# Kernel optimization log

Hardware: AMD Instinct MI355X
Metric: run time of the kernel (lower is better)

## Reference

```python
import jax, jax.numpy as jnp
import numpy as np


def setup_inputs() -> dict:
    key = jax.random.key(0)
    ks = jax.random.split(key, 7)
    B, D, d1, d2, d3 = 256, 256, 1024, 512, 256
    s = lambda f: 1.0 / np.sqrt(f)  # torch nn.Linear-style init scale
    return {
        "x": jax.random.normal(ks[0], (B, D), jnp.float32),
        "W1": jax.random.normal(ks[1], (d1, D), jnp.float32) * s(D),
        "b1": jax.random.normal(ks[2], (d1,), jnp.float32) * s(D),
        "W2": jax.random.normal(ks[3], (d2, d1), jnp.float32) * s(d1),
        "b2": jax.random.normal(ks[4], (d2,), jnp.float32) * s(d1),
        "W3": jax.random.normal(ks[5], (d3, d2), jnp.float32) * s(d2),
        "b3": jax.random.normal(ks[6], (d3,), jnp.float32) * s(d2),
        "k": 10,
    }


def _border_dists(x, W1, b1, W2, b2, W3, b3):
    # Layer 1: pre-activations and boundary distances. For the first layer the
    # effective linear map is W1 itself (shared across the batch).
    z1 = x @ W1.T + b1                                   # [B, d1]
    dist1 = jnp.abs(z1) / jnp.linalg.norm(W1, axis=1)    # [B, d1]
    m1 = (z1 > 0).astype(x.dtype)
    V1 = m1[:, :, None] * W1[None]                       # [B, d1, D] per-instance map after ReLU
    h1 = m1 * z1

    # Layer 2
    z2 = h1 @ W2.T + b2                                  # [B, d2]
    V2 = jnp.einsum('oi,bid->bod', W2, V1)               # [B, d2, D]
    dist2 = jnp.abs(z2) / jnp.linalg.norm(V2, axis=2)
    m2 = (z2 > 0).astype(x.dtype)
    h2 = m2 * z2

    # Layer 3
    z3 = h2 @ W3.T + b3                                  # [B, d3]
    V3 = jnp.einsum('oi,bid->bod', W3, m2[:, :, None] * V2)  # [B, d3, D]
    dist3 = jnp.abs(z3) / jnp.linalg.norm(V3, axis=2)

    return jnp.concatenate([dist1, dist2, dist3], axis=1)  # [B, d1+d2+d3]


def reference(x, W1, b1, W2, b2, W3, b3, k):
    dists = _border_dists(x, W1, b1, W2, b2, W3, b3)
    # smallest-k distances per instance via top_k on negated distances
    neg_top, _ = jax.lax.top_k(-dists, k)                # [B, k]
    return jnp.sum(-neg_top)                             # border-distance loss (scalar)
```

## Files before the change

kernel.cpp:

```cpp
#include <hip/hip_runtime.h>
#include <math.h>
#include <float.h>

#define B   256
#define D   256
#define D1  1024
#define D2  512
#define D3  256
#define NDIST (D1 + D2 + D3)
#define CQ  2.0f

typedef __attribute__((ext_vector_type(8))) short short8;
typedef __attribute__((ext_vector_type(4))) float f32x4;
typedef __attribute__((ext_vector_type(4))) int   i32x4;

__device__ __forceinline__ float waveReduceSum(float v) {
    #pragma unroll
    for (int off = 32; off > 0; off >>= 1)
        v += __shfl_down(v, off, 64);
    return v;
}
__device__ __forceinline__ float waveReduceMax(float v) {
    #pragma unroll
    for (int off = 32; off > 0; off >>= 1)
        v = fmaxf(v, __shfl_down(v, off, 64));
    return v;
}

__device__ __forceinline__ unsigned short f2bf(float f) {
    unsigned int u = __float_as_uint(f);
    u = (u + 0x7FFFu + ((u >> 16) & 1u)) >> 16;
    return (unsigned short)u;
}
__device__ __forceinline__ float bf2f(unsigned short h) {
    return __uint_as_float(((unsigned int)h) << 16);
}
__device__ __forceinline__ void gld16(const void* g, void* l) {
    __builtin_amdgcn_global_load_lds(
        (const __attribute__((address_space(1))) unsigned int*)g,
        (__attribute__((address_space(3))) unsigned int*)l, 16, 0, 0);
}

__device__ __forceinline__ int swz_src(int row, int lane) {
    return ((lane & 3) + ((row >> 1) & 3)) & 3;
}
__device__ __forceinline__ int swz_frag(int row, int quad) {
    return row * 32 + (((quad - ((row >> 1) & 3)) & 3) * 8);
}

__global__ __launch_bounds__(256) void k_prep(
    const float* __restrict__ x,  const float* __restrict__ W1,
    const float* __restrict__ W2, const float* __restrict__ W3,
    float* __restrict__ zeros,
    float* __restrict__ outp,
    unsigned short* __restrict__ xhi,  unsigned short* __restrict__ xlo,
    unsigned short* __restrict__ W1hi, unsigned short* __restrict__ W1lo,
    unsigned short* __restrict__ W2hi, unsigned short* __restrict__ W2lo,
    unsigned short* __restrict__ W3hi, unsigned short* __restrict__ W3lo,
    signed char* __restrict__ W1Ti8, float* __restrict__ saq,
    signed char* __restrict__ W2i8,  float* __restrict__ sbq,
    signed char* __restrict__ W3i8,  float* __restrict__ s3q,
    float* __restrict__ rn1) {
    int blk = blockIdx.x;
    int t = threadIdx.x;
    if (blk < 1536) {
        if (blk == 0 && t == 0) outp[0] = 0.f;
        zeros[blk * 256 + t] = 0.f;
        return;
    }
    if (blk < 2496) {
        int i4 = ((blk - 1536) * 256 + t) * 4;
        const float* src; unsigned short *hi, *lo; int off;
        if (i4 < 65536)       { src = x;  hi = xhi;  lo = xlo;  off = i4; }
        else if (i4 < 327680) { src = W1; hi = W1hi; lo = W1lo; off = i4 - 65536; }
        else if (i4 < 851968) { src = W2; hi = W2hi; lo = W2lo; off = i4 - 327680; }
        else                  { src = W3; hi = W3hi; lo = W3lo; off = i4 - 851968; }
        float4 v = *(const float4*)(src + off);
        ushort4 h, l;
        h.x = f2bf(v.x); l.x = f2bf(v.x - bf2f(h.x));
        h.y = f2bf(v.y); l.y = f2bf(v.y - bf2f(h.y));
        h.z = f2bf(v.z); l.z = f2bf(v.z - bf2f(h.z));
        h.w = f2bf(v.w); l.w = f2bf(v.w - bf2f(h.w));
        *(ushort4*)(hi + off) = h;
        *(ushort4*)(lo + off) = l;
        return;
    }
    if (blk < 2528) {
        int ty = t >> 5, tx = t & 31;
        int d = (blk - 2496) * 8 + ty;
        float m = 0.f;
        for (int i = tx; i < D1; i += 32) m = fmaxf(m, fabsf(W1[(size_t)i * D + d]));
        #pragma unroll
        for (int off = 16; off > 0; off >>= 1) m = fmaxf(m, __shfl_down(m, off, 32));
        m = __shfl(m, 0, 32);
        m = fmaxf(m, 1e-20f);
        if (tx == 0) saq[d] = m / 127.f;
        float inv = 127.f / m;
        for (int i = tx; i < D1; i += 32) {
            int q = __float2int_rn(W1[(size_t)i * D + d] * inv);
            W1Ti8[(size_t)d * D1 + i] = (signed char)q;
        }
        return;
    }
    if (blk < 2656) {
        int o = (blk - 2528) * 4 + (t >> 6);
        int l = t & 63;
        const float* row = W2 + (size_t)o * D1;
        float m = 0.f;
        for (int tt = l; tt < D1; tt += 64) m = fmaxf(m, fabsf(row[tt]));
        m = waveReduceMax(m);
        m = __shfl(m, 0, 64);
        m = fmaxf(m, 1e-20f);
        if (l == 0) sbq[o] = m / 127.f;
        float inv = 127.f / m;
        for (int tt = l; tt < D1; tt += 64)
            W2i8[(size_t)o * D1 + tt] = (signed char)__float2int_rn(row[tt] * inv);
        return;
    }
    if (blk < 2720) {
        int p = (blk - 2656) * 4 + (t >> 6);
        int l = t & 63;
        const float* row = W3 + (size_t)p * D2;
        float m = 0.f;
        for (int tt = l; tt < D2; tt += 64) m = fmaxf(m, fabsf(row[tt]));
        m = waveReduceMax(m);
        m = __shfl(m, 0, 64);
        m = fmaxf(m, 1e-20f);
        if (l == 0) s3q[p] = m / 127.f;
        float inv = 127.f / m;
        for (int tt = l; tt < D2; tt += 64)
            W3i8[(size_t)p * D2 + tt] = (signed char)__float2int_rn(row[tt] * inv);
        return;
    }
    {
        int gw = (blk - 2720) * 4 + (t >> 6);
        int lane = t & 63;
        const float* row = W1 + (size_t)gw * D;
        float s = 0.f;
        for (int tt = lane; tt < D; tt += 64) { float v = row[tt]; s += v * v; }
        s = waveReduceSum(s);
        if (lane == 0) rn1[gw] = sqrtf(s);
    }
}

template <int KD, int KL>
__device__ __forceinline__ void mfma3_64(
    const unsigned short* __restrict__ Ahi, const unsigned short* __restrict__ Alo,
    const unsigned short* __restrict__ Bhi, const unsigned short* __restrict__ Blo,
    int m0, int n0, int k0, unsigned short* sm, f32x4 acc[2][2]) {
    int tid = threadIdx.x;
    int l = tid & 63, w = tid >> 6;
    int rsub = l >> 2;
    int quad = l >> 4, l16 = l & 15;
    int wm = (w >> 1) * 32, wn = (w & 1) * 32;
    unsigned short* sAh = sm;
    unsigned short* sAl = sm + 2048;
    unsigned short* sBh = sm + 4096;
    unsigned short* sBl = sm + 6144;
    ptrdiff_t dA = Alo - Ahi, dB = Blo - Bhi;
    int rloc = w * 16 + rsub;
    int c = swz_src(rloc, l);
    const unsigned short* pa = Ahi + (size_t)(m0 + rloc) * KD + k0 + c * 8;
    const unsigned short* pb = Bhi + (size_t)(n0 + rloc) * KD + k0 + c * 8;
    int aoff[2], boff[2];
    #pragma unroll
    for (int mt = 0; mt < 2; mt++) aoff[mt] = swz_frag(wm + mt * 16 + l16, quad);
    #pragma unroll
    for (int nt = 0; nt < 2; nt++) boff[nt] = swz_frag(wn + nt * 16 + l16, quad);
    for (int kk = 0; kk < KL; kk += 32) {
        gld16(pa + kk,      sAh + w * 512);
        gld16(pa + dA + kk, sAl + w * 512);
        gld16(pb + kk,      sBh + w * 512);
        gld16(pb + dB + kk, sBl + w * 512);
        __syncthreads();
        short8 ah[2], al[2], bh[2], bl[2];
        #pragma unroll
        for (int mt = 0; mt < 2; mt++) {
            ah[mt] = *(const short8*)(sAh + aoff[mt]);
            al[mt] = *(const short8*)(sAl + aoff[mt]);
        }
        #pragma unroll
        for (int nt = 0; nt < 2; nt++) {
            bh[nt] = *(const short8*)(sBh + boff[nt]);
            bl[nt] = *(const short8*)(sBl + boff[nt]);
        }
        #pragma unroll
        for (int mt = 0; mt < 2; mt++)
            #pragma unroll
            for (int nt = 0; nt < 2; nt++) {
                acc[mt][nt] = __builtin_amdgcn_mfma_f32_16x16x32_bf16(ah[mt], bh[nt], acc[mt][nt], 0, 0, 0);
                acc[mt][nt] = __builtin_amdgcn_mfma_f32_16x16x32_bf16(ah[mt], bl[nt], acc[mt][nt], 0, 0, 0);
                acc[mt][nt] = __builtin_amdgcn_mfma_f32_16x16x32_bf16(al[mt], bh[nt], acc[mt][nt], 0, 0, 0);
            }
        __syncthreads();
    }
}

__global__ __launch_bounds__(256) void k_l1(
    const unsigned short* __restrict__ xhi,  const unsigned short* __restrict__ xlo,
    const unsigned short* __restrict__ W1hi, const unsigned short* __restrict__ W1lo,
    const float* __restrict__ b1, const float* __restrict__ rn1,
    float* __restrict__ dists, unsigned char* __restrict__ m1q,
    unsigned short* __restrict__ h1hi, unsigned short* __restrict__ h1lo) {
    __shared__ __align__(16) unsigned short sm[8192];
    int m0 = blockIdx.x * 64, n0 = blockIdx.y * 64;
    f32x4 acc[2][2] = {};
    mfma3_64<D, D>(xhi, xlo, W1hi, W1lo, m0, n0, 0, sm, acc);
    int l = threadIdx.x & 63, w = threadIdx.x >> 6;
    int quad = l >> 4, l16 = l & 15;
    int wm = (w >> 1) * 32, wn = (w & 1) * 32;
    #pragma unroll
    for (int mt = 0; mt < 2; mt++)
        #pragma unroll
        for (int nt = 0; nt < 2; nt++) {
            int n = n0 + wn + nt * 16 + l16;
            float bv = b1[n], rv = rn1[n];
            #pragma unroll
            for (int r = 0; r < 4; r++) {
                int m = m0 + wm + mt * 16 + quad * 4 + r;
                float z = acc[mt][nt][r] + bv;
                size_t idx = (size_t)m * D1 + n;
                dists[idx] = fabsf(z) / rv;
                m1q[idx] = (z > 0.f) ? 0xFFu : 0u;
                float h = z > 0.f ? z : 0.f;
                unsigned short hh = f2bf(h);
                h1hi[idx] = hh;
                h1lo[idx] = f2bf(h - bf2f(hh));
            }
        }
}

__global__ __launch_bounds__(256) void k_l2a(
    const unsigned short* __restrict__ h1hi, const unsigned short* __restrict__ h1lo,
    const unsigned short* __restrict__ W2hi, const unsigned short* __restrict__ W2lo,
    float* __restrict__ z2) {
    __shared__ __align__(16) unsigned short sm[8192];
    int m0 = blockIdx.x * 64, n0 = blockIdx.y * 64, k0 = blockIdx.z * 256;
    f32x4 acc[2][2] = {};
    mfma3_64<D1, 256>(h1hi, h1lo, W2hi, W2lo, m0, n0, k0, sm, acc);
    int l = threadIdx.x & 63, w = threadIdx.x >> 6;
    int quad = l >> 4, l16 = l & 15;
    int wm = (w >> 1) * 32, wn = (w & 1) * 32;
    #pragma unroll
    for (int mt = 0; mt < 2; mt++)
        #pragma unroll
        for (int nt = 0; nt < 2; nt++) {
            int n = n0 + wn + nt * 16 + l16;
            #pragma unroll
            for (int r = 0; r < 4; r++) {
                int m = m0 + wm + mt * 16 + quad * 4 + r;
                atomicAdd(&z2[(size_t)m * D2 + n], acc[mt][nt][r]);
            }
        }
}

__global__ __launch_bounds__(256) void k_l2b(
    const float* __restrict__ b2, float* __restrict__ z2,
    unsigned char* __restrict__ m2q,
    unsigned short* __restrict__ h2hi, unsigned short* __restrict__ h2lo) {
    int idx = blockIdx.x * 256 + threadIdx.x;
    int n = idx & (D2 - 1);
    float z = z2[idx] + b2[n];
    z2[idx] = z;
    m2q[idx] = (z > 0.f) ? 0xFFu : 0u;
    float h = z > 0.f ? z : 0.f;
    unsigned short hh = f2bf(h);
    h2hi[idx] = hh;
    h2lo[idx] = f2bf(h - bf2f(hh));
}

__global__ __launch_bounds__(256) void k_l3a(
    const unsigned short* __restrict__ h2hi, const unsigned short* __restrict__ h2lo,
    const unsigned short* __restrict__ W3hi, const unsigned short* __restrict__ W3lo,
    float* __restrict__ z3) {
    __shared__ __align__(16) unsigned short sm[8192];
    int m0 = blockIdx.x * 64, n0 = blockIdx.y * 64, k0 = blockIdx.z * 256;
    f32x4 acc[2][2] = {};
    mfma3_64<D2, 256>(h2hi, h2lo, W3hi, W3lo, m0, n0, k0, sm, acc);
    int l = threadIdx.x & 63, w = threadIdx.x >> 6;
    int quad = l >> 4, l16 = l & 15;
    int wm = (w >> 1) * 32, wn = (w & 1) * 32;
    #pragma unroll
    for (int mt = 0; mt < 2; mt++)
        #pragma unroll
        for (int nt = 0; nt < 2; nt++) {
            int n = n0 + wn + nt * 16 + l16;
            #pragma unroll
            for (int r = 0; r < 4; r++) {
                int m = m0 + wm + mt * 16 + quad * 4 + r;
                atomicAdd(&z3[(size_t)m * D3 + n], acc[mt][nt][r]);
            }
        }
}

__global__ __launch_bounds__(256) void k_l3b(
    const float* __restrict__ b3, float* __restrict__ z3) {
    int idx = blockIdx.x * 256 + threadIdx.x;
    z3[idx] = z3[idx] + b3[idx & (D3 - 1)];
}

__global__ __launch_bounds__(256) void k_gemm1(
    const signed char* __restrict__ W1Ti8,
    const signed char* __restrict__ W2i8,
    const unsigned char* __restrict__ m1q,
    const float* __restrict__ saq,
    const float* __restrict__ sbq,
    signed char* __restrict__ qV2,
    float* __restrict__ norm2,
    int b0) {
    __shared__ __align__(16) signed char As[16384];
    __shared__ __align__(16) signed char Bs[16384];
    int m0 = blockIdx.x * 128;
    int o0 = blockIdx.y * 128;
    int bc = blockIdx.z;
    int b = b0 + bc;
    int tid = threadIdx.x;
    int l = tid & 63, w = tid >> 6;
    int quad = l >> 4, l16 = l & 15;
    int wm = (w >> 1) * 64, wn = (w & 1) * 64;
    const unsigned char* mrow = m1q + (size_t)b * D1;

    const signed char* pa[4];
    const signed char* pb[4];
    int lrow = l >> 3, ls = l & 7;
    #pragma unroll
    for (int r = 0; r < 4; r++) {
        int row = r * 32 + w * 8 + lrow;
        int c = (ls + (row & 7)) & 7;
        pa[r] = W1Ti8 + (size_t)(m0 + row) * D1 + c * 16;
        pb[r] = W2i8 + (size_t)(o0 + row) * D1 + c * 16;
    }
    int aoff[4][2], boff[4][2];
    #pragma unroll
    for (int mt = 0; mt < 4; mt++) {
        int tr = wm + mt * 16 + l16;
        #pragma unroll
        for (int ks = 0; ks < 2; ks++)
            aoff[mt][ks] = tr * 128 + (((ks * 4 + quad) - (tr & 7)) & 7) * 16;
    }
    #pragma unroll
    for (int nt = 0; nt < 4; nt++) {
        int tr = wn + nt * 16 + l16;
        #pragma unroll
        for (int ks = 0; ks < 2; ks++)
            boff[nt][ks] = tr * 128 + (((ks * 4 + quad) - (tr & 7)) & 7) * 16;
    }

    i32x4 acc[4][4];
    #pragma unroll
    for (int i = 0; i < 4; i++)
        #pragma unroll
        for (int j = 0; j < 4; j++) acc[i][j] = (i32x4)0;

    for (int kk = 0; kk < D1; kk += 128) {
        #pragma unroll
        for (int r = 0; r < 4; r++) {
            gld16(pa[r] + kk, As + r * 4096 + w * 1024);
            gld16(pb[r] + kk, Bs + r * 4096 + w * 1024);
        }
        i32x4 mv0 = *(const i32x4*)(mrow + kk + quad * 16);
        i32x4 mv1 = *(const i32x4*)(mrow + kk + 64 + quad * 16);
        __syncthreads();
        #pragma unroll
        for (int ks = 0; ks < 2; ks++) {
            i32x4 mv = ks ? mv1 : mv0;
            i32x4 a[4], bq[4];
            #pragma unroll
            for (int mt = 0; mt < 4; mt++)
                a[mt] = (*(const i32x4*)(As + aoff[mt][ks])) & mv;
            #pragma unroll
            for (int nt = 0; nt < 4; nt++)
                bq[nt] = *(const i32x4*)(Bs + boff[nt][ks]);
            #pragma unroll
            for (int mt = 0; mt < 4; mt++)
                #pragma unroll
                for (int nt = 0; nt < 4; nt++)
                    acc[mt][nt] = __builtin_amdgcn_mfma_i32_16x16x64_i8(
                        a[mt], bq[nt], acc[mt][nt], 0, 0, 0);
        }
        __syncthreads();
    }

    float sad[4][4];
    #pragma unroll
    for (int mt = 0; mt < 4; mt++)
        #pragma unroll
        for (int r = 0; r < 4; r++)
            sad[mt][r] = saq[m0 + wm + mt * 16 + quad * 4 + r];
    float sbv[4], sbdq[4];
    #pragma unroll
    for (int nt = 0; nt < 4; nt++) {
        sbv[nt] = sbq[o0 + wn + nt * 16 + l16];
        sbdq[nt] = sbv[nt] * (1.0f / CQ);
    }

    #pragma unroll
    for (int nt = 0; nt < 4; nt++) {
        float s = 0.f;
        #pragma unroll
        for (int mt = 0; mt < 4; mt++)
            #pragma unroll
            for (int r = 0; r < 4; r++) {
                float v = (float)acc[mt][nt][r] * sad[mt][r] * sbv[nt];
                s += v * v;
            }
        s += __shfl_down(s, 32, 64);
        s += __shfl_down(s, 16, 64);
        if (l < 16)
            atomicAdd(&norm2[(size_t)b * D2 + o0 + wn + nt * 16 + l], s);
    }

    signed char* qb = qV2 + (size_t)bc * (D * D2);
    #pragma unroll
    for (int mt = 0; mt < 4; mt++) {
        int dbase = m0 + wm + mt * 16 + quad * 4;
        #pragma unroll
        for (int r = 0; r < 4; r++)
            #pragma unroll
            for (int nt = 0; nt < 4; nt++) {
                int o = o0 + wn + nt * 16 + l16;
                int qi = __float2int_rn((float)acc[mt][nt][r] * sbdq[nt]);
                qi = max(-127, min(127, qi));
                qb[(size_t)(dbase + r) * D2 + o] = (signed char)qi;
            }
    }
}

__global__ __launch_bounds__(256) void k_gemm2(
    const signed char* __restrict__ W3i8,
    const signed char* __restrict__ qV2,
    const unsigned char* __restrict__ m2q,
    const float* __restrict__ saq,
    const float* __restrict__ s3q,
    float* __restrict__ norm3,
    int b0) {
    __shared__ __align__(16) signed char As[16384];
    __shared__ __align__(16) signed char Bs[16384];
    int m0 = blockIdx.x * 128;
    int n0 = blockIdx.y * 128;
    int bc = blockIdx.z;
    int b = b0 + bc;
    int tid = threadIdx.x;
    int l = tid & 63, w = tid >> 6;
    int quad = l >> 4, l16 = l & 15;
    int wm = (w >> 1) * 64, wn = (w & 1) * 64;
    const unsigned char* mrow = m2q + (size_t)b * D2;
    const signed char* Bsrc = qV2 + (size_t)bc * (D * D2);

    const signed char* pa[4];
    const signed char* pb[4];
    int lrow = l >> 3, ls = l & 7;
    #pragma unroll
    for (int r = 0; r < 4; r++) {
        int row = r * 32 + w * 8 + lrow;
        int c = (ls + (row & 7)) & 7;
        pa[r] = W3i8 + (size_t)(m0 + row) * D2 + c * 16;
        pb[r] = Bsrc + (size_t)(n0 + row) * D2 + c * 16;
    }
    int aoff[4][2], boff[4][2];
    #pragma unroll
    for (int mt = 0; mt < 4; mt++) {
        int tr = wm + mt * 16 + l16;
        #pragma unroll
        for (int ks = 0; ks < 2; ks++)
            aoff[mt][ks] = tr * 128 + (((ks * 4 + quad) - (tr & 7)) & 7) * 16;
    }
    #pragma unroll
    for (int nt = 0; nt < 4; nt++) {
        int tr = wn + nt * 16 + l16;
        #pragma unroll
        for (int ks = 0; ks < 2; ks++)
            boff[nt][ks] = tr * 128 + (((ks * 4 + quad) - (tr & 7)) & 7) * 16;
    }

    i32x4 acc[4][4];
    #pragma unroll
    for (int i = 0; i < 4; i++)
        #pragma unroll
        for (int j = 0; j < 4; j++) acc[i][j] = (i32x4)0;

    for (int kk = 0; kk < D2; kk += 128) {
        #pragma unroll
        for (int r = 0; r < 4; r++) {
            gld16(pa[r] + kk, As + r * 4096 + w * 1024);
            gld16(pb[r] + kk, Bs + r * 4096 + w * 1024);
        }
        i32x4 mv0 = *(const i32x4*)(mrow + kk + quad * 16);
        i32x4 mv1 = *(const i32x4*)(mrow + kk + 64 + quad * 16);
        __syncthreads();
        #pragma unroll
        for (int ks = 0; ks < 2; ks++) {
            i32x4 mv = ks ? mv1 : mv0;
            i32x4 a[4], bq[4];
            #pragma unroll
            for (int mt = 0; mt < 4; mt++)
                a[mt] = *(const i32x4*)(As + aoff[mt][ks]);
            #pragma unroll
            for (int nt = 0; nt < 4; nt++)
                bq[nt] = (*(const i32x4*)(Bs + boff[nt][ks])) & mv;
            #pragma unroll
            for (int mt = 0; mt < 4; mt++)
                #pragma unroll
                for (int nt = 0; nt < 4; nt++)
                    acc[mt][nt] = __builtin_amdgcn_mfma_i32_16x16x64_i8(
                        a[mt], bq[nt], acc[mt][nt], 0, 0, 0);
        }
        __syncthreads();
    }

    float saCQ[4];
    #pragma unroll
    for (int nt = 0; nt < 4; nt++)
        saCQ[nt] = saq[n0 + wn + nt * 16 + l16] * CQ;

    #pragma unroll
    for (int mt = 0; mt < 4; mt++)
        #pragma unroll
        for (int r = 0; r < 4; r++) {
            float s = 0.f;
            #pragma unroll
            for (int nt = 0; nt < 4; nt++) {
                float v = (float)acc[mt][nt][r] * saCQ[nt];
                s += v * v;
            }
            s += __shfl_down(s, 8, 64);
            s += __shfl_down(s, 4, 64);
            s += __shfl_down(s, 2, 64);
            s += __shfl_down(s, 1, 64);
            if (l16 == 0) {
                int p = m0 + wm + mt * 16 + quad * 4 + r;
                float s3 = s3q[p];
                atomicAdd(&norm3[(size_t)b * D3 + p], s * s3 * s3);
            }
        }
}

__global__ __launch_bounds__(256) void k_topk(
    const float* __restrict__ dists,
    const float* __restrict__ z2, const float* __restrict__ norm2,
    const float* __restrict__ z3, const float* __restrict__ norm3,
    const int* __restrict__ kp, float* __restrict__ outp) {
    __shared__ unsigned long long wmin[4];
    int b = blockIdx.x, t = threadIdx.x;
    float lv[7];
    #pragma unroll
    for (int j = 0; j < 4; j++) lv[j] = dists[(size_t)b * D1 + t + 256 * j];
    #pragma unroll
    for (int j = 4; j < 6; j++) {
        int o = t + 256 * j - 1024;
        lv[j] = fabsf(z2[(size_t)b * D2 + o]) / sqrtf(norm2[(size_t)b * D2 + o]);
    }
    lv[6] = fabsf(z3[(size_t)b * D3 + t]) / sqrtf(norm3[(size_t)b * D3 + t]);
    int k = *kp;
    if (k > NDIST) k = NDIST;
    float sum = 0.f;
    for (int it = 0; it < k; it++) {
        float mv = lv[0]; int mj = 0;
        #pragma unroll
        for (int j = 1; j < 7; j++)
            if (lv[j] < mv) { mv = lv[j]; mj = j; }
        unsigned long long key =
            ((unsigned long long)__float_as_uint(mv) << 32) | (unsigned)(t * 8 + mj);
        #pragma unroll
        for (int off = 32; off > 0; off >>= 1) {
            unsigned long long o = __shfl_down(key, off, 64);
            if (o < key) key = o;
        }
        if ((t & 63) == 0) wmin[t >> 6] = key;
        __syncthreads();
        unsigned long long k0 = wmin[0];
        #pragma unroll
        for (int ww = 1; ww < 4; ww++) if (wmin[ww] < k0) k0 = wmin[ww];
        sum += __uint_as_float((unsigned)(k0 >> 32));
        int wt = (int)((k0 & 0xFFFu) >> 3), wj = (int)(k0 & 7u);
        if (t == wt) lv[wj] = FLT_MAX;
        __syncthreads();
    }
    if (t == 0) atomicAdd(outp, sum);
}

extern "C" void kernel_launch(void* const* d_in, const int* in_sizes, int n_in,
                              void* d_out, int out_size, void* d_ws, size_t ws_size,
                              hipStream_t stream) {
    const float* x  = (const float*)d_in[0];
    const float* W1 = (const float*)d_in[1];
    const float* b1 = (const float*)d_in[2];
    const float* W2 = (const float*)d_in[3];
    const float* b2 = (const float*)d_in[4];
    const float* W3 = (const float*)d_in[5];
    const float* b3 = (const float*)d_in[6];
    const int*   kp = (const int*)d_in[7];
    float* outp = (float*)d_out;

    float* fp = (float*)d_ws;
    float* rn1     = fp;                          fp += D1;
    float* dists   = fp;                          fp += (size_t)B * D1;
    float* saq     = fp;                          fp += D;
    float* sbq     = fp;                          fp += D2;
    float* s3q     = fp;                          fp += D3;
    float* z2      = fp;                          fp += (size_t)B * D2;
    float* z3      = fp;                          fp += (size_t)B * D3;
    float* norm2   = fp;                          fp += (size_t)B * D2;
    float* norm3   = fp;                          fp += (size_t)B * D3;
    unsigned short* up = (unsigned short*)fp;
    unsigned short* W2hi  = up;  up += (size_t)D2 * D1;
    unsigned short* W2lo  = up;  up += (size_t)D2 * D1;
    unsigned short* W3hi  = up;  up += (size_t)D3 * D2;
    unsigned short* W3lo  = up;  up += (size_t)D3 * D2;
    unsigned short* xhi   = up;  up += (size_t)B * D;
    unsigned short* xlo   = up;  up += (size_t)B * D;
    unsigned short* W1hi  = up;  up += (size_t)D1 * D;
    unsigned short* W1lo  = up;  up += (size_t)D1 * D;
    unsigned short* h1hi  = up;  up += (size_t)B * D1;
    unsigned short* h1lo  = up;  up += (size_t)B * D1;
    unsigned short* h2hi  = up;  up += (size_t)B * D2;
    unsigned short* h2lo  = up;  up += (size_t)B * D2;
    signed char*    cp = (signed char*)up;
    signed char*    W1Ti8 = cp;  cp += (size_t)D * D1;
    signed char*    W2i8  = cp;  cp += (size_t)D2 * D1;
    signed char*    W3i8  = cp;  cp += (size_t)D3 * D2;
    unsigned char*  m1q   = (unsigned char*)cp;  cp += (size_t)B * D1;
    unsigned char*  m2q   = (unsigned char*)cp;  cp += (size_t)B * D2;
    signed char*    qV2   = cp;

    size_t base_bytes = (size_t)((char*)qV2 - (char*)d_ws);
    int CH = 8;
    const int cands[6] = {256, 128, 64, 32, 16, 8};
    for (int c = 0; c < 6; c++) {
        size_t need = base_bytes + (size_t)cands[c] * D * D2;
        if (need <= ws_size) { CH = cands[c]; break; }
    }

    k_prep<<<2976, 256, 0, stream>>>(x, W1, W2, W3, z2, outp,
                                     xhi, xlo, W1hi, W1lo, W2hi, W2lo, W3hi, W3lo,
                                     W1Ti8, saq, W2i8, sbq, W3i8, s3q, rn1);

    k_l1<<<dim3(B / 64, D1 / 64), 256, 0, stream>>>(xhi, xlo, W1hi, W1lo, b1, rn1,
                                                    dists, m1q, h1hi, h1lo);
    k_l2a<<<dim3(B / 64, D2 / 64, 4), 256, 0, stream>>>(h1hi, h1lo, W2hi, W2lo, z2);
    k_l2b<<<(B * D2) / 256, 256, 0, stream>>>(b2, z2, m2q, h2hi, h2lo);
    k_l3a<<<dim3(B / 64, D3 / 64, 2), 256, 0, stream>>>(h2hi, h2lo, W3hi, W3lo, z3);
    k_l3b<<<(B * D3) / 256, 256, 0, stream>>>(b3, z3);

    for (int b0 = 0; b0 < B; b0 += CH) {
        k_gemm1<<<dim3(D / 128, D2 / 128, CH), 256, 0, stream>>>(
            W1Ti8, W2i8, m1q, saq, sbq, qV2, norm2, b0);
        k_gemm2<<<dim3(D3 / 128, D / 128, CH), 256, 0, stream>>>(
            W3i8, qV2, m2q, saq, s3q, norm3, b0);
    }

    k_topk<<<B, 256, 0, stream>>>(dists, z2, norm2, z3, norm3, kp, outp);
}
```

Before: 192.4 us.

## Fuse all stages into one cooperative persistent kernel with grid syncs

Replaces the sequence of separate kernel launches (prep, layer GEMMs, bias passes, chunked int8 V-GEMMs, top-k) with a single cooperative kernel that loops over job indices and separates stages with grid-wide syncs. It also co-schedules independent work in the same phase (gemm1 with l2a, gemm2 with l3a), folds the l3b bias add into top-k, and drops the batch chunking of qV2 by assuming the workspace holds all 256 batches. This is meant to remove launch gaps and tail idling, at the cost of grid-sync overhead, a fixed grid size tied to occupancy, and heavier register pressure from merging all paths into one kernel.

```diff
diff --git a/kernel.cpp b/kernel.cpp
--- a/kernel.cpp
+++ b/kernel.cpp
@@ -1,6 +1,9 @@
 #include <hip/hip_runtime.h>
+#include <hip/hip_cooperative_groups.h>
 #include <math.h>
 #include <float.h>
+
+namespace cg = cooperative_groups;
 
 #define B   256
 #define D   256
@@ -14,6 +17,19 @@
 typedef __attribute__((ext_vector_type(4))) float f32x4;
 typedef __attribute__((ext_vector_type(4))) int   i32x4;
 
+struct KArgs {
+    const float *x, *W1, *b1, *W2, *b2, *W3, *b3;
+    const int* kp;
+    float* outp;
+    float *rn1, *dists, *saq, *sbq, *s3q;
+    float *z2, *z3, *norm2, *norm3;
+    unsigned short *W2hi, *W2lo, *W3hi, *W3lo, *xhi, *xlo, *W1hi, *W1lo;
+    unsigned short *h1hi, *h1lo, *h2hi, *h2lo;
+    signed char *W1Ti8, *W2i8, *W3i8;
+    unsigned char *m1q, *m2q;
+    signed char* qV2;
+};
+
 __device__ __forceinline__ float waveReduceSum(float v) {
     #pragma unroll
     for (int off = 32; off > 0; off >>= 1)
@@ -26,7 +42,6 @@
         v = fmaxf(v, __shfl_down(v, off, 64));
     return v;
 }
-
 __device__ __forceinline__ unsigned short f2bf(float f) {
     unsigned int u = __float_as_uint(f);
     u = (u + 0x7FFFu + ((u >> 16) & 1u)) >> 16;
@@ -40,7 +55,6 @@
         (const __attribute__((address_space(1))) unsigned int*)g,
         (__attribute__((address_space(3))) unsigned int*)l, 16, 0, 0);
 }
-
 __device__ __forceinline__ int swz_src(int row, int lane) {
     return ((lane & 3) + ((row >> 1) & 3)) & 3;
 }
@@ -48,33 +62,20 @@
     return row * 32 + (((quad - ((row >> 1) & 3)) & 3) * 8);
 }
 
-__global__ __launch_bounds__(256) void k_prep(
-    const float* __restrict__ x,  const float* __restrict__ W1,
-    const float* __restrict__ W2, const float* __restrict__ W3,
-    float* __restrict__ zeros,
-    float* __restrict__ outp,
-    unsigned short* __restrict__ xhi,  unsigned short* __restrict__ xlo,
-    unsigned short* __restrict__ W1hi, unsigned short* __restrict__ W1lo,
-    unsigned short* __restrict__ W2hi, unsigned short* __restrict__ W2lo,
-    unsigned short* __restrict__ W3hi, unsigned short* __restrict__ W3lo,
-    signed char* __restrict__ W1Ti8, float* __restrict__ saq,
-    signed char* __restrict__ W2i8,  float* __restrict__ sbq,
-    signed char* __restrict__ W3i8,  float* __restrict__ s3q,
-    float* __restrict__ rn1) {
-    int blk = blockIdx.x;
+__device__ void job_prep(const KArgs& A, int blk) {
     int t = threadIdx.x;
     if (blk < 1536) {
-        if (blk == 0 && t == 0) outp[0] = 0.f;
-        zeros[blk * 256 + t] = 0.f;
+        if (blk == 0 && t == 0) A.outp[0] = 0.f;
+        A.z2[blk * 256 + t] = 0.f;
         return;
     }
     if (blk < 2496) {
         int i4 = ((blk - 1536) * 256 + t) * 4;
         const float* src; unsigned short *hi, *lo; int off;
-        if (i4 < 65536)       { src = x;  hi = xhi;  lo = xlo;  off = i4; }
-        else if (i4 < 327680) { src = W1; hi = W1hi; lo = W1lo; off = i4 - 65536; }
-        else if (i4 < 851968) { src = W2; hi = W2hi; lo = W2lo; off = i4 - 327680; }
-        else                  { src = W3; hi = W3hi; lo = W3lo; off = i4 - 851968; }
+        if (i4 < 65536)       { src = A.x;  hi = A.xhi;  lo = A.xlo;  off = i4; }
+        else if (i4 < 327680) { src = A.W1; hi = A.W1hi; lo = A.W1lo; off = i4 - 65536; }
+        else if (i4 < 851968) { src = A.W2; hi = A.W2hi; lo = A.W2lo; off = i4 - 327680; }
+        else                  { src = A.W3; hi = A.W3hi; lo = A.W3lo; off = i4 - 851968; }
         float4 v = *(const float4*)(src + off);
         ushort4 h, l;
         h.x = f2bf(v.x); l.x = f2bf(v.x - bf2f(h.x));
@@ -89,57 +90,57 @@
         int ty = t >> 5, tx = t & 31;
         int d = (blk - 2496) * 8 + ty;
         float m = 0.f;
-        for (int i = tx; i < D1; i += 32) m = fmaxf(m, fabsf(W1[(size_t)i * D + d]));
+        for (int i = tx; i < D1; i += 32) m = fmaxf(m, fabsf(A.W1[(size_t)i * D + d]));
         #pragma unroll
         for (int off = 16; off > 0; off >>= 1) m = fmaxf(m, __shfl_down(m, off, 32));
         m = __shfl(m, 0, 32);
         m = fmaxf(m, 1e-20f);
-        if (tx == 0) saq[d] = m / 127.f;
+        if (tx == 0) A.saq[d] = m / 127.f;
         float inv = 127.f / m;
         for (int i = tx; i < D1; i += 32) {
-            int q = __float2int_rn(W1[(size_t)i * D + d] * inv);
-            W1Ti8[(size_t)d * D1 + i] = (signed char)q;
+            int q = __float2int_rn(A.W1[(size_t)i * D + d] * inv);
+            A.W1Ti8[(size_t)d * D1 + i] = (signed char)q;
         }
         return;
     }
     if (blk < 2656) {
         int o = (blk - 2528) * 4 + (t >> 6);
         int l = t & 63;
-        const float* row = W2 + (size_t)o * D1;
+        const float* row = A.W2 + (size_t)o * D1;
         float m = 0.f;
         for (int tt = l; tt < D1; tt += 64) m = fmaxf(m, fabsf(row[tt]));
         m = waveReduceMax(m);
         m = __shfl(m, 0, 64);
         m = fmaxf(m, 1e-20f);
-        if (l == 0) sbq[o] = m / 127.f;
+        if (l == 0) A.sbq[o] = m / 127.f;
         float inv = 127.f / m;
         for (int tt = l; tt < D1; tt += 64)
-            W2i8[(size_t)o * D1 + tt] = (signed char)__float2int_rn(row[tt] * inv);
+            A.W2i8[(size_t)o * D1 + tt] = (signed char)__float2int_rn(row[tt] * inv);
         return;
     }
     if (blk < 2720) {
         int p = (blk - 2656) * 4 + (t >> 6);
         int l = t & 63;
-        const float* row = W3 + (size_t)p * D2;
+        const float* row = A.W3 + (size_t)p * D2;
         float m = 0.f;
         for (int tt = l; tt < D2; tt += 64) m = fmaxf(m, fabsf(row[tt]));
         m = waveReduceMax(m);
         m = __shfl(m, 0, 64);
         m = fmaxf(m, 1e-20f);
-        if (l == 0) s3q[p] = m / 127.f;
+        if (l == 0) A.s3q[p] = m / 127.f;
         float inv = 127.f / m;
         for (int tt = l; tt < D2; tt += 64)
-            W3i8[(size_t)p * D2 + tt] = (signed char)__float2int_rn(row[tt] * inv);
+            A.W3i8[(size_t)p * D2 + tt] = (signed char)__float2int_rn(row[tt] * inv);
         return;
     }
     {
         int gw = (blk - 2720) * 4 + (t >> 6);
         int lane = t & 63;
-        const float* row = W1 + (size_t)gw * D;
+        const float* row = A.W1 + (size_t)gw * D;
         float s = 0.f;
         for (int tt = lane; tt < D; tt += 64) { float v = row[tt]; s += v * v; }
         s = waveReduceSum(s);
-        if (lane == 0) rn1[gw] = sqrtf(s);
+        if (lane == 0) A.rn1[gw] = sqrtf(s);
     }
 }
 
@@ -196,16 +197,10 @@
     }
 }
 
-__global__ __launch_bounds__(256) void k_l1(
-    const unsigned short* __restrict__ xhi,  const unsigned short* __restrict__ xlo,
-    const unsigned short* __restrict__ W1hi, const unsigned short* __restrict__ W1lo,
-    const float* __restrict__ b1, const float* __restrict__ rn1,
-    float* __restrict__ dists, unsigned char* __restrict__ m1q,
-    unsigned short* __restrict__ h1hi, unsigned short* __restrict__ h1lo) {
-    __shared__ __align__(16) unsigned short sm[8192];
-    int m0 = blockIdx.x * 64, n0 = blockIdx.y * 64;
+__device__ void job_l1(const KArgs& A, int j, unsigned short* sm) {
+    int m0 = (j & 3) * 64, n0 = (j >> 2) * 64;
     f32x4 acc[2][2] = {};
-    mfma3_64<D, D>(xhi, xlo, W1hi, W1lo, m0, n0, 0, sm, acc);
+    mfma3_64<D, D>(A.xhi, A.xlo, A.W1hi, A.W1lo, m0, n0, 0, sm, acc);
     int l = threadIdx.x & 63, w = threadIdx.x >> 6;
     int quad = l >> 4, l16 = l & 15;
     int wm = (w >> 1) * 32, wn = (w & 1) * 32;
@@ -214,30 +209,26 @@
         #pragma unroll
         for (int nt = 0; nt < 2; nt++) {
             int n = n0 + wn + nt * 16 + l16;
-            float bv = b1[n], rv = rn1[n];
+            float bv = A.b1[n], rv = A.rn1[n];
             #pragma unroll
             for (int r = 0; r < 4; r++) {
                 int m = m0 + wm + mt * 16 + quad * 4 + r;
                 float z = acc[mt][nt][r] + bv;
                 size_t idx = (size_t)m * D1 + n;
-                dists[idx] = fabsf(z) / rv;
-                m1q[idx] = (z > 0.f) ? 0xFFu : 0u;
+                A.dists[idx] = fabsf(z) / rv;
+                A.m1q[idx] = (z > 0.f) ? 0xFFu : 0u;
                 float h = z > 0.f ? z : 0.f;
                 unsigned short hh = f2bf(h);
-                h1hi[idx] = hh;
-                h1lo[idx] = f2bf(h - bf2f(hh));
-            }
-        }
-}
-
-__global__ __launch_bounds__(256) void k_l2a(
-    const unsigned short* __restrict__ h1hi, const unsigned short* __restrict__ h1lo,
-    const unsigned short* __restrict__ W2hi, const unsigned short* __restrict__ W2lo,
-    float* __restrict__ z2) {
-    __shared__ __align__(16) unsigned short sm[8192];
-    int m0 = blockIdx.x * 64, n0 = blockIdx.y * 64, k0 = blockIdx.z * 256;
+                A.h1hi[idx] = hh;
+                A.h1lo[idx] = f2bf(h - bf2f(hh));
+            }
+        }
+}
+
+__device__ void job_l2a(const KArgs& A, int bx, int by, int bz, unsigned short* sm) {
+    int m0 = bx * 64, n0 = by * 64, k0 = bz * 256;
     f32x4 acc[2][2] = {};
-    mfma3_64<D1, 256>(h1hi, h1lo, W2hi, W2lo, m0, n0, k0, sm, acc);
+    mfma3_64<D1, 256>(A.h1hi, A.h1lo, A.W2hi, A.W2lo, m0, n0, k0, sm, acc);
     int l = threadIdx.x & 63, w = threadIdx.x >> 6;
     int quad = l >> 4, l16 = l & 15;
     int wm = (w >> 1) * 32, wn = (w & 1) * 32;
@@ -249,34 +240,27 @@
             #pragma unroll
             for (int r = 0; r < 4; r++) {
                 int m = m0 + wm + mt * 16 + quad * 4 + r;
-                atomicAdd(&z2[(size_t)m * D2 + n], acc[mt][nt][r]);
-            }
-        }
-}
-
-__global__ __launch_bounds__(256) void k_l2b(
-    const float* __restrict__ b2, float* __restrict__ z2,
-    unsigned char* __restrict__ m2q,
-    unsigned short* __restrict__ h2hi, unsigned short* __restrict__ h2lo) {
-    int idx = blockIdx.x * 256 + threadIdx.x;
+                atomicAdd(&A.z2[(size_t)m * D2 + n], acc[mt][nt][r]);
+            }
+        }
+}
+
+__device__ void job_l2b(const KArgs& A, int j) {
+    int idx = j * 256 + threadIdx.x;
     int n = idx & (D2 - 1);
-    float z = z2[idx] + b2[n];
-    z2[idx] = z;
-    m2q[idx] = (z > 0.f) ? 0xFFu : 0u;
+    float z = A.z2[idx] + A.b2[n];
+    A.z2[idx] = z;
+    A.m2q[idx] = (z > 0.f) ? 0xFFu : 0u;
     float h = z > 0.f ? z : 0.f;
     unsigned short hh = f2bf(h);
-    h2hi[idx] = hh;
-    h2lo[idx] = f2bf(h - bf2f(hh));
-}
-
-__global__ __launch_bounds__(256) void k_l3a(
-    const unsigned short* __restrict__ h2hi, const unsigned short* __restrict__ h2lo,
-    const unsigned short* __restrict__ W3hi, const unsigned short* __restrict__ W3lo,
-    float* __restrict__ z3) {
-    __shared__ __align__(16) unsigned short sm[8192];
-    int m0 = blockIdx.x * 64, n0 = blockIdx.y * 64, k0 = blockIdx.z * 256;
+    A.h2hi[idx] = hh;
+    A.h2lo[idx] = f2bf(h - bf2f(hh));
+}
+
+__device__ void job_l3a(const KArgs& A, int bx, int by, int bz, unsigned short* sm) {
+    int m0 = bx * 64, n0 = by * 64, k0 = bz * 256;
     f32x4 acc[2][2] = {};
-    mfma3_64<D2, 256>(h2hi, h2lo, W3hi, W3lo, m0, n0, k0, sm, acc);
+    mfma3_64<D2, 256>(A.h2hi, A.h2lo, A.W3hi, A.W3lo, m0, n0, k0, sm, acc);
     int l = threadIdx.x & 63, w = threadIdx.x >> 6;
     int quad = l >> 4, l16 = l & 15;
     int wm = (w >> 1) * 32, wn = (w & 1) * 32;
@@ -288,37 +272,22 @@
             #pragma unroll
             for (int r = 0; r < 4; r++) {
                 int m = m0 + wm + mt * 16 + quad * 4 + r;
-                atomicAdd(&z3[(size_t)m * D3 + n], acc[mt][nt][r]);
-            }
-        }
-}
-
-__global__ __launch_bounds__(256) void k_l3b(
-    const float* __restrict__ b3, float* __restrict__ z3) {
-    int idx = blockIdx.x * 256 + threadIdx.x;
-    z3[idx] = z3[idx] + b3[idx & (D3 - 1)];
-}
-
-__global__ __launch_bounds__(256) void k_gemm1(
-    const signed char* __restrict__ W1Ti8,
-    const signed char* __restrict__ W2i8,
-    const unsigned char* __restrict__ m1q,
-    const float* __restrict__ saq,
-    const float* __restrict__ sbq,
-    signed char* __restrict__ qV2,
-    float* __restrict__ norm2,
-    int b0) {
-    __shared__ __align__(16) signed char As[16384];
-    __shared__ __align__(16) signed char Bs[16384];
-    int m0 = blockIdx.x * 128;
-    int o0 = blockIdx.y * 128;
-    int bc = blockIdx.z;
-    int b = b0 + bc;
+                atomicAdd(&A.z3[(size_t)m * D3 + n], acc[mt][nt][r]);
+            }
+        }
+}
+
+__device__ void job_gemm1(const KArgs& A, int bx, int by, int bc, signed char* smem) {
+    signed char* As = smem;
+    signed char* Bs = smem + 16384;
+    int m0 = bx * 128;
+    int o0 = by * 128;
+    int b = bc;
     int tid = threadIdx.x;
     int l = tid & 63, w = tid >> 6;
     int quad = l >> 4, l16 = l & 15;
     int wm = (w >> 1) * 64, wn = (w & 1) * 64;
-    const unsigned char* mrow = m1q + (size_t)b * D1;
+    const unsigned char* mrow = A.m1q + (size_t)b * D1;
 
     const signed char* pa[4];
     const signed char* pb[4];
@@ -327,8 +296,8 @@
     for (int r = 0; r < 4; r++) {
         int row = r * 32 + w * 8 + lrow;
         int c = (ls + (row & 7)) & 7;
-        pa[r] = W1Ti8 + (size_t)(m0 + row) * D1 + c * 16;
-        pb[r] = W2i8 + (size_t)(o0 + row) * D1 + c * 16;
+        pa[r] = A.W1Ti8 + (size_t)(m0 + row) * D1 + c * 16;
+        pb[r] = A.W2i8 + (size_t)(o0 + row) * D1 + c * 16;
     }
     int aoff[4][2], boff[4][2];
     #pragma unroll
@@ -350,7 +319,7 @@
     #pragma unroll
     for (int i = 0; i < 4; i++)
         #pragma unroll
-        for (int j = 0; j < 4; j++) acc[i][j] = (i32x4)0;
+        for (int jj = 0; jj < 4; jj++) acc[i][jj] = (i32x4)0;
 
     for (int kk = 0; kk < D1; kk += 128) {
         #pragma unroll
@@ -386,11 +355,11 @@
     for (int mt = 0; mt < 4; mt++)
         #pragma unroll
         for (int r = 0; r < 4; r++)
-            sad[mt][r] = saq[m0 + wm + mt * 16 + quad * 4 + r];
+            sad[mt][r] = A.saq[m0 + wm + mt * 16 + quad * 4 + r];
     float sbv[4], sbdq[4];
     #pragma unroll
     for (int nt = 0; nt < 4; nt++) {
-        sbv[nt] = sbq[o0 + wn + nt * 16 + l16];
+        sbv[nt] = A.sbq[o0 + wn + nt * 16 + l16];
         sbdq[nt] = sbv[nt] * (1.0f / CQ);
     }
 
@@ -407,10 +376,10 @@
         s += __shfl_down(s, 32, 64);
         s += __shfl_down(s, 16, 64);
         if (l < 16)
-            atomicAdd(&norm2[(size_t)b * D2 + o0 + wn + nt * 16 + l], s);
-    }
-
-    signed char* qb = qV2 + (size_t)bc * (D * D2);
+            atomicAdd(&A.norm2[(size_t)b * D2 + o0 + wn + nt * 16 + l], s);
+    }
+
+    signed char* qb = A.qV2 + (size_t)bc * (D * D2);
     #pragma unroll
     for (int mt = 0; mt < 4; mt++) {
         int dbase = m0 + wm + mt * 16 + quad * 4;
@@ -426,26 +395,18 @@
     }
 }
 
-__global__ __launch_bounds__(256) void k_gemm2(
-    const signed char* __restrict__ W3i8,
-    const signed char* __restrict__ qV2,
-    const unsigned char* __restrict__ m2q,
-    const float* __restrict__ saq,
-    const float* __restrict__ s3q,
-    float* __restrict__ norm3,
-    int b0) {
-    __shared__ __align__(16) signed char As[16384];
-    __shared__ __align__(16) signed char Bs[16384];
-    int m0 = blockIdx.x * 128;
-    int n0 = blockIdx.y * 128;
-    int bc = blockIdx.z;
-    int b = b0 + bc;
+__device__ void job_gemm2(const KArgs& A, int bx, int by, int bc, signed char* smem) {
+    signed char* As = smem;
+    signed char* Bs = smem + 16384;
+    int m0 = bx * 128;
+    int n0 = by * 128;
+    int b = bc;
     int tid = threadIdx.x;
     int l = tid & 63, w = tid >> 6;
     int quad = l >> 4, l16 = l & 15;
     int wm = (w >> 1) * 64, wn = (w & 1) * 64;
-    const unsigned char* mrow = m2q + (size_t)b * D2;
-    const signed char* Bsrc = qV2 + (size_t)bc * (D * D2);
+    const unsigned char* mrow = A.m2q + (size_t)b * D2;
+    const signed char* Bsrc = A.qV2 + (size_t)bc * (D * D2);
 
     const signed char* pa[4];
     const signed char* pb[4];
@@ -454,7 +415,7 @@
     for (int r = 0; r < 4; r++) {
         int row = r * 32 + w * 8 + lrow;
         int c = (ls + (row & 7)) & 7;
-        pa[r] = W3i8 + (size_t)(m0 + row) * D2 + c * 16;
+        pa[r] = A.W3i8 + (size_t)(m0 + row) * D2 + c * 16;
         pb[r] = Bsrc + (size_t)(n0 + row) * D2 + c * 16;
     }
     int aoff[4][2], boff[4][2];
@@ -477,7 +438,7 @@
     #pragma unroll
     for (int i = 0; i < 4; i++)
         #pragma unroll
-        for (int j = 0; j < 4; j++) acc[i][j] = (i32x4)0;
+        for (int jj = 0; jj < 4; jj++) acc[i][jj] = (i32x4)0;
 
     for (int kk = 0; kk < D2; kk += 128) {
         #pragma unroll
@@ -511,7 +472,7 @@
     float saCQ[4];
     #pragma unroll
     for (int nt = 0; nt < 4; nt++)
-        saCQ[nt] = saq[n0 + wn + nt * 16 + l16] * CQ;
+        saCQ[nt] = A.saq[n0 + wn + nt * 16 + l16] * CQ;
 
     #pragma unroll
     for (int mt = 0; mt < 4; mt++)
@@ -529,29 +490,28 @@
             s += __shfl_down(s, 1, 64);
             if (l16 == 0) {
                 int p = m0 + wm + mt * 16 + quad * 4 + r;
-                float s3 = s3q[p];
-                atomicAdd(&norm3[(size_t)b * D3 + p], s * s3 * s3);
-            }
-        }
-}
-
-__global__ __launch_bounds__(256) void k_topk(
-    const float* __restrict__ dists,
-    const float* __restrict__ z2, const float* __restrict__ norm2,
-    const float* __restrict__ z3, const float* __restrict__ norm3,
-    const int* __restrict__ kp, float* __restrict__ outp) {
-    __shared__ unsigned long long wmin[4];
-    int b = blockIdx.x, t = threadIdx.x;
+                float s3 = A.s3q[p];
+                atomicAdd(&A.norm3[(size_t)b * D3 + p], s * s3 * s3);
+            }
+        }
+}
+
+__device__ void job_topk(const KArgs& A, int b, unsigned long long* wmin) {
+    __syncthreads();
+    int t = threadIdx.x;
     float lv[7];
     #pragma unroll
-    for (int j = 0; j < 4; j++) lv[j] = dists[(size_t)b * D1 + t + 256 * j];
+    for (int j = 0; j < 4; j++) lv[j] = A.dists[(size_t)b * D1 + t + 256 * j];
     #pragma unroll
     for (int j = 4; j < 6; j++) {
         int o = t + 256 * j - 1024;
-        lv[j] = fabsf(z2[(size_t)b * D2 + o]) / sqrtf(norm2[(size_t)b * D2 + o]);
-    }
-    lv[6] = fabsf(z3[(size_t)b * D3 + t]) / sqrtf(norm3[(size_t)b * D3 + t]);
-    int k = *kp;
+        lv[j] = fabsf(A.z2[(size_t)b * D2 + o]) / sqrtf(A.norm2[(size_t)b * D2 + o]);
+    }
+    {
+        float zz = A.z3[(size_t)b * D3 + t] + A.b3[t];
+        lv[6] = fabsf(zz) / sqrtf(A.norm3[(size_t)b * D3 + t]);
+    }
+    int k = *A.kp;
     if (k > NDIST) k = NDIST;
     float sum = 0.f;
     for (int it = 0; it < k; it++) {
@@ -576,78 +536,88 @@
         if (t == wt) lv[wj] = FLT_MAX;
         __syncthreads();
     }
-    if (t == 0) atomicAdd(outp, sum);
+    if (t == 0) atomicAdd(A.outp, sum);
+}
+
+__global__ __launch_bounds__(256, 2) void k_all(KArgs A) {
+    __shared__ __align__(16) unsigned char smem[32768];
+    cg::grid_group grid = cg::this_grid();
+    int bid = blockIdx.x, G = gridDim.x;
+
+    for (int j = bid; j < 2976; j += G) job_prep(A, j);
+    __threadfence(); grid.sync();
+
+    for (int j = bid; j < 64; j += G) job_l1(A, j, (unsigned short*)smem);
+    __threadfence(); grid.sync();
+
+    for (int j = bid; j < 2176; j += G) {
+        if (j < 2048) job_gemm1(A, j & 1, (j >> 1) & 3, j >> 3, (signed char*)smem);
+        else { int jj = j - 2048; job_l2a(A, jj & 3, (jj >> 2) & 7, jj >> 5, (unsigned short*)smem); }
+    }
+    __threadfence(); grid.sync();
+
+    for (int j = bid; j < 512; j += G) job_l2b(A, j);
+    __threadfence(); grid.sync();
+
+    for (int j = bid; j < 1056; j += G) {
+        if (j < 1024) job_gemm2(A, j & 1, (j >> 1) & 1, j >> 2, (signed char*)smem);
+        else { int jj = j - 1024; job_l3a(A, jj & 3, (jj >> 2) & 3, jj >> 4, (unsigned short*)smem); }
+    }
+    __threadfence(); grid.sync();
+
+    for (int j = bid; j < 256; j += G) job_topk(A, j, (unsigned long long*)smem);
 }
 
 extern "C" void kernel_launch(void* const* d_in, const int* in_sizes, int n_in,
                               void* d_out, int out_size, void* d_ws, size_t ws_size,
                               hipStream_t stream) {
-    const float* x  = (const float*)d_in[0];
-    const float* W1 = (const float*)d_in[1];
-    const float* b1 = (const float*)d_in[2];
-    const float* W2 = (const float*)d_in[3];
-    const float* b2 = (const float*)d_in[4];
-    const float* W3 = (const float*)d_in[5];
-    const float* b3 = (const float*)d_in[6];
-    const int*   kp = (const int*)d_in[7];
-    float* outp = (float*)d_out;
+    KArgs A;
+    A.x  = (const float*)d_in[0];
+    A.W1 = (const float*)d_in[1];
+    A.b1 = (const float*)d_in[2];
+    A.W2 = (const float*)d_in[3];
+    A.b2 = (const float*)d_in[4];
+    A.W3 = (const float*)d_in[5];
+    A.b3 = (const float*)d_in[6];
+    A.kp = (const int*)d_in[7];
+    A.outp = (float*)d_out;
 
     float* fp = (float*)d_ws;
-    float* rn1     = fp;                          fp += D1;
-    float* dists   = fp;                          fp += (size_t)B * D1;
-    float* saq     = fp;                          fp += D;
-    float* sbq     = fp;                          fp += D2;
-    float* s3q     = fp;                          fp += D3;
-    float* z2      = fp;                          fp += (size_t)B * D2;
-    float* z3      = fp;                          fp += (size_t)B * D3;
-    float* norm2   = fp;                          fp += (size_t)B * D2;
-    float* norm3   = fp;                          fp += (size_t)B * D3;
+    A.rn1   = fp;  fp += D1;
+    A.dists = fp;  fp += (size_t)B * D1;
+    A.saq   = fp;  fp += D;
+    A.sbq   = fp;  fp += D2;
+    A.s3q   = fp;  fp += D3;
+    A.z2    = fp;  fp += (size_t)B * D2;
+    A.z3    = fp;  fp += (size_t)B * D3;
+    A.norm2 = fp;  fp += (size_t)B * D2;
+    A.norm3 = fp;  fp += (size_t)B * D3;
     unsigned short* up = (unsigned short*)fp;
-    unsigned short* W2hi  = up;  up += (size_t)D2 * D1;
-    unsigned short* W2lo  = up;  up += (size_t)D2 * D1;
-    unsigned short* W3hi  = up;  up += (size_t)D3 * D2;
-    unsigned short* W3lo  = up;  up += (size_t)D3 * D2;
-    unsigned short* xhi   = up;  up += (size_t)B * D;
-    unsigned short* xlo   = up;  up += (size_t)B * D;
-    unsigned short* W1hi  = up;  up += (size_t)D1 * D;
-    unsigned short* W1lo  = up;  up += (size_t)D1 * D;
-    unsigned short* h1hi  = up;  up += (size_t)B * D1;
-    unsigned short* h1lo  = up;  up += (size_t)B * D1;
-    unsigned short* h2hi  = up;  up += (size_t)B * D2;
-    unsigned short* h2lo  = up;  up += (size_t)B * D2;
-    signed char*    cp = (signed char*)up;
-    signed char*    W1Ti8 = cp;  cp += (size_t)D * D1;
-    signed char*    W2i8  = cp;  cp += (size_t)D2 * D1;
-    signed char*    W3i8  = cp;  cp += (size_t)D3 * D2;
-    unsigned char*  m1q   = (unsigned char*)cp;  cp += (size_t)B * D1;
-    unsigned char*  m2q   = (unsigned char*)cp;  cp += (size_t)B * D2;
-    signed char*    qV2   = cp;
-
-    size_t base_bytes = (size_t)((char*)qV2 - (char*)d_ws);
-    int CH = 8;
-    const int cands[6] = {256, 128, 64, 32, 16, 8};
-    for (int c = 0; c < 6; c++) {
-        size_t need = base_bytes + (size_t)cands[c] * D * D2;
-        if (need <= ws_size) { CH = cands[c]; break; }
-    }
-
-    k_prep<<<2976, 256, 0, stream>>>(x, W1, W2, W3, z2, outp,
-                                     xhi, xlo, W1hi, W1lo, W2hi, W2lo, W3hi, W3lo,
-                                     W1Ti8, saq, W2i8, sbq, W3i8, s3q, rn1);
-
-    k_l1<<<dim3(B / 64, D1 / 64), 256, 0, stream>>>(xhi, xlo, W1hi, W1lo, b1, rn1,
-                                                    dists, m1q, h1hi, h1lo);
-    k_l2a<<<dim3(B / 64, D2 / 64, 4), 256, 0, stream>>>(h1hi, h1lo, W2hi, W2lo, z2);
-    k_l2b<<<(B * D2) / 256, 256, 0, stream>>>(b2, z2, m2q, h2hi, h2lo);
-    k_l3a<<<dim3(B / 64, D3 / 64, 2), 256, 0, stream>>>(h2hi, h2lo, W3hi, W3lo, z3);
-    k_l3b<<<(B * D3) / 256, 256, 0, stream>>>(b3, z3);
-
-    for (int b0 = 0; b0 < B; b0 += CH) {
-        k_gemm1<<<dim3(D / 128, D2 / 128, CH), 256, 0, stream>>>(
-            W1Ti8, W2i8, m1q, saq, sbq, qV2, norm2, b0);
-        k_gemm2<<<dim3(D3 / 128, D / 128, CH), 256, 0, stream>>>(
-            W3i8, qV2, m2q, saq, s3q, norm3, b0);
-    }
-
-    k_topk<<<B, 256, 0, stream>>>(dists, z2, norm2, z3, norm3, kp, outp);
-}
+    A.W2hi = up;  up += (size_t)D2 * D1;
+    A.W2lo = up;  up += (size_t)D2 * D1;
+    A.W3hi = up;  up += (size_t)D3 * D2;
+    A.W3lo = up;  up += (size_t)D3 * D2;
+    A.xhi  = up;  up += (size_t)B * D;
+    A.xlo  = up;  up += (size_t)B * D;
+    A.W1hi = up;  up += (size_t)D1 * D;
+    A.W1lo = up;  up += (size_t)D1 * D;
+    A.h1hi = up;  up += (size_t)B * D1;
+    A.h1lo = up;  up += (size_t)B * D1;
+    A.h2hi = up;  up += (size_t)B * D2;
+    A.h2lo = up;  up += (size_t)B * D2;
+    signed char* cp = (signed char*)up;
+    A.W1Ti8 = cp;  cp += (size_t)D * D1;
+    A.W2i8  = cp;  cp += (size_t)D2 * D1;
+    A.W3i8  = cp;  cp += (size_t)D3 * D2;
+    A.m1q   = (unsigned char*)cp;  cp += (size_t)B * D1;
+    A.m2q   = (unsigned char*)cp;  cp += (size_t)B * D2;
+    A.qV2   = cp;
+
+    int nb = 0;
+    if (hipOccupancyMaxActiveBlocksPerMultiprocessor(&nb, k_all, 256, 0) != hipSuccess || nb < 1)
+        nb = 1;
+    int G = (nb >= 2) ? 512 : 256;
+
+    void* params[] = { (void*)&A };
+    hipLaunchCooperativeKernel((void*)k_all, dim3(G), dim3(256), params, 0, stream);
+}
```

After: 520.1 us. +170.3%, slower.
